# Optimization experiments

Hardware: AMD Instinct MI355X
Metric: run time of the kernel (lower is better)

The kernel has to match this reference:

```python
import jax, jax.numpy as jnp
import numpy as np

B, L, F, DM, H, DFF, NL, PRED = 8, 1000, 7, 512, 8, 2048, 4, 50
DK = DM // H           # head dim 64
P = DK // 4            # learned-mask proj dim 16
EPS = 1e-5
SCALE = 1.0 / float(np.sqrt(DK))


def _ln(x, g, b):
    m = jnp.mean(x, -1, keepdims=True)
    v = jnp.mean((x - m) ** 2, -1, keepdims=True)
    return (x - m) / jnp.sqrt(v + EPS) * g + b


def _make_pe():
    pos = np.arange(L, dtype=np.float32)[:, None]
    div = np.exp(np.arange(0, DM, 2, dtype=np.float32) * (-np.log(10000.0) / DM))
    pe = np.zeros((L, DM), dtype=np.float32)
    pe[:, 0::2] = np.sin(pos * div)
    pe[:, 1::2] = np.cos(pos * div)
    return jnp.asarray(pe)


def setup_inputs() -> dict:
    key = jax.random.key(0)
    ks = iter(jax.random.split(key, 40))
    def w(shape, s=0.02):
        return jax.random.normal(next(ks), shape, jnp.float32) * s
    return {
        "x": jax.random.normal(next(ks), (B, L, F), jnp.float32),
        "emb_w": w((F, DM)), "emb_b": jnp.zeros((DM,), jnp.float32),
        "pe": _make_pe(),
        "Wq": w((NL, DM, DM)), "bq": jnp.zeros((NL, DM), jnp.float32),
        "Wk": w((NL, DM, DM)), "bk": jnp.zeros((NL, DM), jnp.float32),
        "Wv": w((NL, DM, DM)), "bv": jnp.zeros((NL, DM), jnp.float32),
        "Wo": w((NL, DM, DM)), "bo": jnp.zeros((NL, DM), jnp.float32),
        "W1": w((NL, DM, DFF)), "b1": jnp.zeros((NL, DFF), jnp.float32),
        "W2": w((NL, DFF, DM)), "b2": jnp.zeros((NL, DM), jnp.float32),
        "g1": jnp.ones((NL, DM), jnp.float32), "be1": jnp.zeros((NL, DM), jnp.float32),
        "g2": jnp.ones((NL, DM), jnp.float32), "be2": jnp.zeros((NL, DM), jnp.float32),
        "lm_qw": w((DK, P)), "lm_qb": jnp.zeros((P,), jnp.float32),
        "lm_kw": w((DK, P)), "lm_kb": jnp.zeros((P,), jnp.float32),
        "gn": jnp.ones((DM,), jnp.float32), "bn": jnp.zeros((DM,), jnp.float32),
        "fc_w": w((DM, PRED)), "fc_b": jnp.zeros((PRED,), jnp.float32),
    }


def reference(x, emb_w, emb_b, pe, Wq, bq, Wk, bk, Wv, bv, Wo, bo,
              W1, b1, W2, b2, g1, be1, g2, be2,
              lm_qw, lm_qb, lm_kw, lm_kb, gn, bn, fc_w, fc_b):
    # eval mode: dropout = identity
    h = x @ emb_w + emb_b + pe[None]                 # [B,L,DM]
    for i in range(NL):
        q = (h @ Wq[i] + bq[i]).reshape(B, L, H, DK)
        k = (h @ Wk[i] + bk[i]).reshape(B, L, H, DK)
        v = (h @ Wv[i] + bv[i]).reshape(B, L, H, DK)
        scores = jnp.einsum('blhd,bshd->bhls', q, k) * SCALE
        # shared LearnedMask: per-head Q/K projection to P dims, tanh bias
        qp = q @ lm_qw + lm_qb                       # [B,L,H,P]
        kp = k @ lm_kw + lm_kb                       # [B,S,H,P]
        scores = scores + jnp.tanh(jnp.einsum('blhp,bshp->bhls', qp, kp))
        attn = jax.nn.softmax(scores, axis=-1)       # mask_flag=False: no mask
        ctx = jnp.einsum('bhls,bshd->blhd', attn, v).reshape(B, L, DM)
        h = _ln(h + ctx @ Wo[i] + bo[i], g1[i], be1[i])
        y = jax.nn.relu(h @ W1[i] + b1[i]) @ W2[i] + b2[i]
        h2 = _ln(h + y, g2[i], be2[i])
        h = _ln(h2 + y, g2[i], be2[i])               # module applies norm2 twice
    h = _ln(h, gn, bn)                               # Encoder final norm
    return h[:, -1, :] @ fc_w + fc_b                 # [B, PRED]
```

## Files before the change

### kernel.cpp

```cpp
#include <hip/hip_runtime.h>
#include <math.h>

#define B_    8
#define L_    1000
#define F_    7
#define DM_   512
#define H_    8
#define DFF_  2048
#define NL_   4
#define PRED_ 50
#define DK_   64
#define P_    16
#define EPS_  1e-5f
#define QKVS  1792

#define L2E_   1.4426950408889634f
#define C_QS   0.18033688011112042f
#define BS_QP  2.8853900817779268f
#define SHFT_  24.0f

typedef unsigned short u16;
typedef __bf16 bf16x8 __attribute__((ext_vector_type(8)));
typedef float  f32x4  __attribute__((ext_vector_type(4)));

__device__ inline float wave_reduce_sum(float x) {
#pragma unroll
  for (int off = 32; off >= 1; off >>= 1) x += __shfl_xor(x, off, 64);
  return x;
}
__device__ inline u16 f2bf(float f) {
  unsigned int u = __float_as_uint(f);
  unsigned int r = u + 0x7FFFu + ((u >> 16) & 1u);
  return (u16)(r >> 16);
}
__device__ inline unsigned int pack2(float a, float b) {
  return (unsigned int)f2bf(a) | ((unsigned int)f2bf(b) << 16);
}
__device__ inline float bf2f(u16 u) { return __uint_as_float(((unsigned int)u) << 16); }
__device__ inline float fexp2(float x) { return __builtin_amdgcn_exp2f(x); }
__device__ inline float frcp(float x) { return __builtin_amdgcn_rcpf(x); }

union bfrag { bf16x8 b; uint4 q; u16 u[8]; };

__device__ inline void gload16(const u16* g, u16* l) {
  __builtin_amdgcn_global_load_lds(
      (const __attribute__((address_space(1))) void*)g,
      (__attribute__((address_space(3))) void*)l, 16, 0, 0);
}

__global__ __launch_bounds__(256)
void transpose_w(const float* __restrict__ in, u16* __restrict__ out,
                 int K, int N, size_t in_lstride, size_t out_lstride,
                 int row_off, int out_ld) {
  __shared__ float tile[32][33];
  int z = blockIdx.z;
  int kk0 = blockIdx.y * 32, nn0 = blockIdx.x * 32;
  int tx = threadIdx.x & 31, ty = threadIdx.x >> 5;
  const float* ip = in + z * in_lstride;
  u16* op = out + z * out_lstride;
#pragma unroll
  for (int i = 0; i < 4; i++)
    tile[ty + i * 8][tx] = ip[(size_t)(kk0 + ty + i * 8) * N + nn0 + tx];
  __syncthreads();
#pragma unroll
  for (int i = 0; i < 4; i++)
    op[(size_t)(row_off + nn0 + ty + i * 8) * out_ld + kk0 + tx] = f2bf(tile[tx][ty + i * 8]);
}

__global__ __launch_bounds__(256)
void wfuse_kernel(const float* __restrict__ Wq, const float* __restrict__ Wk,
                  const float* __restrict__ lmqw, const float* __restrict__ lmkw,
                  u16* __restrict__ Wt) {
  int hh = blockIdx.x, side = blockIdx.y, layer = blockIdx.z;
  const float* W = (side ? Wk : Wq) + (size_t)layer * 512 * 512;
  const float* lw = side ? lmkw : lmqw;
  float scale = side ? 1.0f : BS_QP;
  __shared__ float lws[64][17];
  int t = threadIdx.x;
  for (int i = t; i < 1024; i += 256) lws[i >> 4][i & 15] = lw[i];
  __syncthreads();
  int p = t & 15, kk = t >> 4;
  u16* orow = Wt + (size_t)layer * QKVS * 512 + (size_t)(1536 + side * 128 + hh * 16 + p) * 512;
  for (int kb = 0; kb < 32; kb++) {
    int k = kb * 16 + kk;
    const float* wr = W + (size_t)k * 512 + hh * 64;
    float acc = 0.f;
#pragma unroll
    for (int d = 0; d < 64; d++) acc = fmaf(wr[d], lws[d][p], acc);
    orow[k] = f2bf(acc * scale);
  }
}

__global__ __launch_bounds__(256)
void concat_bias(const float* __restrict__ bq, const float* __restrict__ bk,
                 const float* __restrict__ bv,
                 const float* __restrict__ lmqw, const float* __restrict__ lmqb,
                 const float* __restrict__ lmkw, const float* __restrict__ lmkb,
                 float* __restrict__ bqkv) {
  int i = blockIdx.x * 256 + threadIdx.x;
  int l = i / QKVS, j = i % QKVS;
  float v;
  if (j < 512) v = bq[l * 512 + j];
  else if (j < 1024) v = bk[l * 512 + j - 512];
  else if (j < 1536) v = bv[l * 512 + j - 1024];
  else if (j < 1664) {
    int hh = (j - 1536) >> 4, p = (j - 1536) & 15;
    float acc = lmqb[p];
#pragma unroll
    for (int d = 0; d < 64; d++) acc = fmaf(bq[l * 512 + hh * 64 + d], lmqw[d * 16 + p], acc);
    v = acc * BS_QP;
  } else {
    int hh = (j - 1664) >> 4, p = (j - 1664) & 15;
    float acc = lmkb[p];
#pragma unroll
    for (int d = 0; d < 64; d++) acc = fmaf(bk[l * 512 + hh * 64 + d], lmkw[d * 16 + p], acc);
    v = acc;
  }
  bqkv[i] = v;
}

__global__ __launch_bounds__(512)
void embed_kernel(const float* __restrict__ x, const float* __restrict__ emb_w,
                  const float* __restrict__ emb_b, const float* __restrict__ pe,
                  u16* __restrict__ h16) {
  int bl = blockIdx.x;
  int l = bl % L_;
  int d = threadIdx.x;
  const float* xr = x + (size_t)bl * F_;
  float acc = emb_b[d] + pe[(size_t)l * DM_ + d];
#pragma unroll
  for (int f = 0; f < F_; f++) acc = fmaf(xr[f], emb_w[f * DM_ + d], acc);
  h16[(size_t)bl * DM_ + d] = f2bf(acc);
}

template<int BN>
__global__ __launch_bounds__(256)
void gemm16(const u16* __restrict__ A, const u16* __restrict__ Bt,
            const float* __restrict__ bias, const u16* __restrict__ resid,
            u16* __restrict__ C16, u16* __restrict__ vtg,
            int M, int K, int N, int relu, int nscale, float sval) {
  constexpr int NTW = BN / 32;
  constexpr int BG  = BN / 32;
  __shared__ u16 As[128 * 64];
  __shared__ u16 Bs[BN * 64];
  int t = threadIdx.x;
  int w = t >> 6, lane = t & 63;
  int wr = w >> 1, wc = w & 1;
  int mloc = lane & 15, quad = lane >> 4;
  int m0 = blockIdx.y * 128, n0 = blockIdx.x * BN;

  const u16* agp[4]; u16* alds[4];
#pragma unroll
  for (int j = 0; j < 4; j++) {
    int r = w * 32 + j * 8 + (lane >> 3);
    int gm = m0 + r; if (gm > M - 1) gm = M - 1;
    int ch = (lane & 7) ^ (r & 7);
    agp[j] = A + (size_t)gm * K + ch * 8;
    alds[j] = As + (w * 32 + j * 8) * 64;
  }
  const u16* bgp[BG]; u16* blds[BG];
#pragma unroll
  for (int j = 0; j < BG; j++) {
    int r = w * (8 * BG) + j * 8 + (lane >> 3);
    int ch = (lane & 7) ^ (r & 7);
    bgp[j] = Bt + (size_t)(n0 + r) * K + ch * 8;
    blds[j] = Bs + (w * (8 * BG) + j * 8) * 64;
  }
  const u16* apt[2][4];
#pragma unroll
  for (int mi = 0; mi < 4; mi++) {
    int tr = wr * 64 + mi * 16 + mloc;
    apt[0][mi] = As + tr * 64 + ((quad ^ (tr & 7)) * 8);
    apt[1][mi] = As + tr * 64 + (((4 + quad) ^ (tr & 7)) * 8);
  }
  const u16* bpt[2][NTW];
#pragma unroll
  for (int nt = 0; nt < NTW; nt++) {
    int tr = wc * (BN / 2) + nt * 16 + mloc;
    bpt[0][nt] = Bs + tr * 64 + ((quad ^ (tr & 7)) * 8);
    bpt[1][nt] = Bs + tr * 64 + (((4 + quad) ^ (tr & 7)) * 8);
  }

  f32x4 acc[4][NTW];
#pragma unroll
  for (int mi = 0; mi < 4; mi++)
#pragma unroll
    for (int nt = 0; nt < NTW; nt++) acc[mi][nt] = (f32x4){0.f, 0.f, 0.f, 0.f};

  for (int k0 = 0; k0 < K; k0 += 64) {
    __syncthreads();
#pragma unroll
    for (int j = 0; j < 4; j++) gload16(agp[j] + k0, alds[j]);
#pragma unroll
    for (int j = 0; j < BG; j++) gload16(bgp[j] + k0, blds[j]);
    __syncthreads();
#pragma unroll
    for (int kc = 0; kc < 2; kc++) {
      bf16x8 af[4], bv[NTW];
#pragma unroll
      for (int mi = 0; mi < 4; mi++) af[mi] = *(const bf16x8*)apt[kc][mi];
#pragma unroll
      for (int nt = 0; nt < NTW; nt++) bv[nt] = *(const bf16x8*)bpt[kc][nt];
#pragma unroll
      for (int mi = 0; mi < 4; mi++)
#pragma unroll
        for (int nt = 0; nt < NTW; nt++)
          acc[mi][nt] = __builtin_amdgcn_mfma_f32_16x16x32_bf16(af[mi], bv[nt], acc[mi][nt], 0, 0, 0);
    }
  }

#pragma unroll
  for (int mi = 0; mi < 4; mi++) {
    int m_r0 = m0 + wr * 64 + mi * 16 + quad * 4;
#pragma unroll
    for (int nt = 0; nt < NTW; nt++) {
      int nbase = n0 + wc * (BN / 2) + nt * 16;
      int n = nbase + mloc;
      if (vtg && nbase >= 1024 && nbase < 1536) {
        if (m_r0 < M) {
          int bb = (m_r0 * 67109) >> 26;
          int ll = m_r0 - bb * 1000;
          int hh2 = (n - 1024) >> 6, dk = n & 63;
          float bn_ = bias[n];
          union { uint2 d; u16 s[4]; } pk;
#pragma unroll
          for (int r = 0; r < 4; r++) pk.s[r] = f2bf(acc[mi][nt][r] + bn_);
          u16* dst = vtg + ((size_t)(bb * 8 + hh2) * 64 + dk) * 1024 + ll;
          *(uint2*)dst = pk.d;
        }
      } else {
        float bn_ = bias[n];
#pragma unroll
        for (int r = 0; r < 4; r++) {
          int m = m_r0 + r;
          if (m >= M) continue;
          size_t crow = (size_t)m * N;
          float vsum = acc[mi][nt][r] + bn_;
          if (resid) vsum += bf2f(resid[crow + n]);
          if (n < nscale) vsum *= sval;
          if (relu) vsum = fmaxf(vsum, 0.f);
          C16[crow + n] = f2bf(vsum);
        }
      }
    }
  }
}

#define KT   64
__global__ __launch_bounds__(256)
void attn_mfma_kernel(const u16* __restrict__ qkv, const u16* __restrict__ vtg,
                      u16* __restrict__ ctx) {
  __shared__ u16 Ks[2 * KT * 64];
  __shared__ u16 Vt[2 * 64 * KT];
  __shared__ u16 Kp[2 * KT * 16];

  int Lid = blockIdx.x;
  int qt = Lid >> 6;
  int bh = ((Lid & 7) << 3) | ((Lid >> 3) & 7);
  int b = bh >> 3, hh = bh & 7;
  int l0 = qt * 64;
  int t = threadIdx.x;
  int wv = t >> 6, lane = t & 63;
  int m = lane & 15, quad = lane >> 4;

  int lq = l0 + wv * 16 + m; if (lq > L_ - 1) lq = L_ - 1;
  const u16* qrow = qkv + (size_t)(b * L_ + lq) * QKVS + hh * DK_;
  bf16x8 qa0 = *(const bf16x8*)(qrow + quad * 8);
  bf16x8 qa1 = *(const bf16x8*)(qrow + 32 + quad * 8);
  bfrag qpa;
  if (quad < 2) {
    qpa.q = *(const uint4*)(qkv + (size_t)(b * L_ + lq) * QKVS + 1536 + hh * P_ + quad * 8);
  } else {
    qpa.q = make_uint4(0u, 0u, 0u, 0u);
  }

  const u16* ks_g = qkv + ((size_t)b * L_ + (t >> 3)) * QKVS + 512 + hh * DK_
                    + ((t & 7) ^ ((t >> 3) & 7)) * 8;
  u16* ks_l = Ks + wv * 512;
  const u16* vt_g = vtg + ((size_t)bh * DK_ + (t >> 3)) * 1024
                    + ((t & 7) ^ ((t >> 3) & 7)) * 8;
  u16* vt_l = Vt + wv * 512;
  const u16* kp_g = qkv + ((size_t)b * L_ + (t >> 1)) * QKVS + 1664 + hh * P_
                    + (t & 1) * 8;
  u16* kp_l = Kp + wv * 512;

  f32x4 O[4];
#pragma unroll
  for (int nt = 0; nt < 4; nt++) O[nt] = (f32x4){0.f, 0.f, 0.f, 0.f};
  float lsum = 0.f;
  const f32x4 zz = (f32x4){0.f, 0.f, 0.f, 0.f};

#pragma unroll
  for (int j = 0; j < 2; j++) {
    gload16(ks_g + (size_t)(j * 32) * QKVS, ks_l + j * 2048);
    gload16(vt_g + (size_t)j * 32 * 1024, vt_l + j * 2048);
  }
  if (wv < 2) gload16(kp_g, kp_l);
  __syncthreads();

  for (int tt = 0; tt < 16; ++tt) {
    const int s0 = tt * KT;
    const int c = tt & 1;
    if (tt < 15) {
      const int sn = s0 + KT, nb = c ^ 1;
#pragma unroll
      for (int j = 0; j < 2; j++) {
        gload16(ks_g + ((size_t)sn + j * 32) * QKVS, ks_l + nb * 4096 + j * 2048);
        gload16(vt_g + sn + (size_t)j * 32 * 1024, vt_l + nb * 4096 + j * 2048);
      }
      if (wv < 2) gload16(kp_g + (size_t)sn * QKVS, kp_l + nb * 1024);
    }

    const u16* Kc = Ks + c * 4096;
    const u16* Vc = Vt + c * 4096;
    const u16* Pc = Kp + c * 1024;

    unsigned pklo[4], pkhi[4];
#pragma unroll
    for (int nt = 0; nt < 4; nt++) {
      const u16* kb = Kc + (nt * 16 + m) * 64;
      int x0 = (quad ^ (m & 7)) * 8;
      int x1 = ((4 + quad) ^ (m & 7)) * 8;
      bf16x8 kf0 = *(const bf16x8*)(kb + x0);
      bf16x8 kf1 = *(const bf16x8*)(kb + x1);
      bf16x8 kpf = *(const bf16x8*)(Pc + (nt * 16 + m) * 16 + (quad & 1) * 8);
      __builtin_amdgcn_s_setprio(1);
      f32x4 sacc = __builtin_amdgcn_mfma_f32_16x16x32_bf16(kf0, qa0, zz, 0, 0, 0);
      sacc = __builtin_amdgcn_mfma_f32_16x16x32_bf16(kf1, qa1, sacc, 0, 0, 0);
      f32x4 macc = __builtin_amdgcn_mfma_f32_16x16x32_bf16(kpf, qpa.b, zz, 0, 0, 0);
      __builtin_amdgcn_s_setprio(0);
      int keyb = s0 + nt * 16 + quad * 4;
      float pv[4];
#pragma unroll
      for (int r = 0; r < 4; r++) {
        float e = fexp2(macc[r]);
        float d = frcp(e + 1.f);
        float th = fmaf(d, -2.f * L2E_, L2E_);
        float s = sacc[r] + th;
        if (keyb + r >= L_) s = -3e38f;
        float p = fexp2(s - SHFT_);
        pv[r] = p;
        lsum += p;
      }
      pklo[nt] = pack2(pv[0], pv[1]);
      pkhi[nt] = pack2(pv[2], pv[3]);
    }

#pragma unroll
    for (int ks = 0; ks < 2; ks++) {
      int sl = m + ((quad & 1) << 5);
      unsigned e0a = (unsigned)__shfl((int)pklo[2 * ks],     sl, 64);
      unsigned e0b = (unsigned)__shfl((int)pklo[2 * ks + 1], sl, 64);
      unsigned e1a = (unsigned)__shfl((int)pkhi[2 * ks],     sl, 64);
      unsigned e1b = (unsigned)__shfl((int)pkhi[2 * ks + 1], sl, 64);
      unsigned o0a = (unsigned)__shfl((int)pklo[2 * ks],     sl + 16, 64);
      unsigned o0b = (unsigned)__shfl((int)pklo[2 * ks + 1], sl + 16, 64);
      unsigned o1a = (unsigned)__shfl((int)pkhi[2 * ks],     sl + 16, 64);
      unsigned o1b = (unsigned)__shfl((int)pkhi[2 * ks + 1], sl + 16, 64);
      bool hi = quad >= 2;
      bfrag af;
      af.q.x = hi ? e0b : e0a;
      af.q.y = hi ? e1b : e1a;
      af.q.z = hi ? o0b : o0a;
      af.q.w = hi ? o1b : o1a;
      __builtin_amdgcn_s_setprio(1);
#pragma unroll
      for (int ntd = 0; ntd < 4; ntd++) {
        const u16* vb = Vc + (ntd * 16 + m) * KT + (((ks * 4 + quad) ^ (m & 7)) * 8);
        O[ntd] = __builtin_amdgcn_mfma_f32_16x16x32_bf16(af.b, *(const bf16x8*)vb, O[ntd], 0, 0, 0);
      }
      __builtin_amdgcn_s_setprio(0);
    }
    if (tt < 15) __syncthreads();
  }

  lsum += __shfl_xor(lsum, 16, 64);
  lsum += __shfl_xor(lsum, 32, 64);
#pragma unroll
  for (int r = 0; r < 4; r++) {
    int l = l0 + wv * 16 + quad * 4 + r;
    if (l >= L_) continue;
    float inv = frcp(__shfl(lsum, quad * 4 + r, 64));
    u16* crow = ctx + ((size_t)(b * L_ + l)) * DM_ + hh * DK_;
#pragma unroll
    for (int nt = 0; nt < 4; nt++) crow[nt * 16 + m] = f2bf(O[nt][r] * inv);
  }
}

__global__ __launch_bounds__(256)
void ln_kernel(const u16* __restrict__ a, const float* __restrict__ g,
               const float* __restrict__ be, u16* __restrict__ o) {
  int row = blockIdx.x;
  int t = threadIdx.x;
  size_t base = (size_t)row * DM_;
  unsigned int av = *(const unsigned int*)(a + base + 2 * t);
  float x0 = bf2f((u16)av), x1 = bf2f((u16)(av >> 16));
  float s = wave_reduce_sum(x0 + x1);
  float ss = wave_reduce_sum(x0 * x0 + x1 * x1);
  __shared__ float sh_s[4], sh_ss[4];
  int wv = t >> 6, lane = t & 63;
  if (lane == 0) { sh_s[wv] = s; sh_ss[wv] = ss; }
  __syncthreads();
  float S = sh_s[0] + sh_s[1] + sh_s[2] + sh_s[3];
  float SS = sh_ss[0] + sh_ss[1] + sh_ss[2] + sh_ss[3];
  float mean = S * (1.0f / DM_);
  float var = SS * (1.0f / DM_) - mean * mean;
  float rstd = rsqrtf(var + EPS_);
  float r0 = (x0 - mean) * rstd * g[2 * t] + be[2 * t];
  float r1 = (x1 - mean) * rstd * g[2 * t + 1] + be[2 * t + 1];
  *(unsigned int*)(o + base + 2 * t) = pack2(r0, r1);
}

__global__ __launch_bounds__(256)
void ln2x_kernel(const u16* __restrict__ hin, const u16* __restrict__ y,
                 const float* __restrict__ g, const float* __restrict__ be,
                 u16* __restrict__ o16) {
  int row = blockIdx.x;
  int t = threadIdx.x;
  size_t base = (size_t)row * DM_;
  unsigned int hv = *(const unsigned int*)(hin + base + 2 * t);
  unsigned int yv = *(const unsigned int*)(y + base + 2 * t);
  float y0 = bf2f((u16)yv), y1 = bf2f((u16)(yv >> 16));
  float x0 = bf2f((u16)hv) + y0, x1 = bf2f((u16)(hv >> 16)) + y1;
  __shared__ float sh_s[4], sh_ss[4];
  int wv = t >> 6, lane = t & 63;
  float g0 = g[2 * t], g1v = g[2 * t + 1], b0 = be[2 * t], b1v = be[2 * t + 1];

  float s = wave_reduce_sum(x0 + x1);
  float ss = wave_reduce_sum(x0 * x0 + x1 * x1);
  if (lane == 0) { sh_s[wv] = s; sh_ss[wv] = ss; }
  __syncthreads();
  float S = sh_s[0] + sh_s[1] + sh_s[2] + sh_s[3];
  float SS = sh_ss[0] + sh_ss[1] + sh_ss[2] + sh_ss[3];
  float mean = S * (1.0f / DM_);
  float var = SS * (1.0f / DM_) - mean * mean;
  float rstd = rsqrtf(var + EPS_);
  float h20 = (x0 - mean) * rstd * g0 + b0 + y0;
  float h21 = (x1 - mean) * rstd * g1v + b1v + y1;
  __syncthreads();

  s = wave_reduce_sum(h20 + h21);
  ss = wave_reduce_sum(h20 * h20 + h21 * h21);
  if (lane == 0) { sh_s[wv] = s; sh_ss[wv] = ss; }
  __syncthreads();
  S = sh_s[0] + sh_s[1] + sh_s[2] + sh_s[3];
  SS = sh_ss[0] + sh_ss[1] + sh_ss[2] + sh_ss[3];
  mean = S * (1.0f / DM_);
  var = SS * (1.0f / DM_) - mean * mean;
  rstd = rsqrtf(var + EPS_);
  float r0 = (h20 - mean) * rstd * g0 + b0;
  float r1 = (h21 - mean) * rstd * g1v + b1v;
  *(unsigned int*)(o16 + base + 2 * t) = pack2(r0, r1);
}

__global__ __launch_bounds__(512)
void final_kernel(const u16* __restrict__ h, const float* __restrict__ gn,
                  const float* __restrict__ bn, const float* __restrict__ fcw,
                  const float* __restrict__ fcb, float* __restrict__ out) {
  int b = blockIdx.x;
  int t = threadIdx.x;
  size_t base = ((size_t)b * L_ + (L_ - 1)) * DM_;
  float x = bf2f(h[base + t]);
  float s = wave_reduce_sum(x);
  float ss = wave_reduce_sum(x * x);
  __shared__ float sh_s[8], sh_ss[8];
  int wv = t >> 6, lane = t & 63;
  if (lane == 0) { sh_s[wv] = s; sh_ss[wv] = ss; }
  __syncthreads();
  float S = 0.f, SS = 0.f;
#pragma unroll
  for (int i = 0; i < 8; i++) { S += sh_s[i]; SS += sh_ss[i]; }
  float mean = S * (1.0f / DM_);
  float var = SS * (1.0f / DM_) - mean * mean;
  float rstd = rsqrtf(var + EPS_);
  __shared__ float hn[DM_];
  hn[t] = (x - mean) * rstd * gn[t] + bn[t];
  __syncthreads();
  if (t < PRED_) {
    float acc = fcb[t];
#pragma unroll 8
    for (int d = 0; d < DM_; d++) acc = fmaf(hn[d], fcw[d * PRED_ + t], acc);
    out[b * PRED_ + t] = acc;
  }
}

extern "C" void kernel_launch(void* const* d_in, const int* in_sizes, int n_in,
                              void* d_out, int out_size, void* d_ws, size_t ws_size,
                              hipStream_t stream) {
  const float* x     = (const float*)d_in[0];
  const float* emb_w = (const float*)d_in[1];
  const float* emb_b = (const float*)d_in[2];
  const float* pe    = (const float*)d_in[3];
  const float* Wq = (const float*)d_in[4];  const float* bq = (const float*)d_in[5];
  const float* Wk = (const float*)d_in[6];  const float* bk = (const float*)d_in[7];
  const float* Wv = (const float*)d_in[8];  const float* bv = (const float*)d_in[9];
  const float* Wo = (const float*)d_in[10]; const float* bo = (const float*)d_in[11];
  const float* W1 = (const float*)d_in[12]; const float* b1 = (const float*)d_in[13];
  const float* W2 = (const float*)d_in[14]; const float* b2 = (const float*)d_in[15];
  const float* g1 = (const float*)d_in[16]; const float* be1 = (const float*)d_in[17];
  const float* g2 = (const float*)d_in[18]; const float* be2 = (const float*)d_in[19];
  const float* lm_qw = (const float*)d_in[20]; const float* lm_qb = (const float*)d_in[21];
  const float* lm_kw = (const float*)d_in[22]; const float* lm_kb = (const float*)d_in[23];
  const float* gn = (const float*)d_in[24]; const float* bn = (const float*)d_in[25];
  const float* fc_w = (const float*)d_in[26]; const float* fc_b = (const float*)d_in[27];
  float* out = (float*)d_out;

  const size_t ROWS = (size_t)B_ * L_;
  u16* qkv16 = (u16*)d_ws;
  u16* ctx16 = qkv16 + ROWS * QKVS;
  u16* ffn1  = qkv16;
  u16* h16   = ctx16 + ROWS * DM_;
  u16* t16   = h16 + ROWS * DM_;
  u16* vtg   = t16 + ROWS * DM_;
  u16* Wqkv_t = vtg + (size_t)64 * 64 * 1024;
  u16* Wo_t   = Wqkv_t + (size_t)NL_ * QKVS * DM_;
  u16* W1_t   = Wo_t + (size_t)NL_ * DM_ * DM_;
  u16* W2_t   = W1_t + (size_t)NL_ * DFF_ * DM_;
  float* bqkv = (float*)(W2_t + (size_t)NL_ * DM_ * DFF_);

  transpose_w<<<dim3(16, 16, NL_), 256, 0, stream>>>(Wq, Wqkv_t, DM_, DM_, (size_t)DM_ * DM_, (size_t)QKVS * DM_, 0, DM_);
  transpose_w<<<dim3(16, 16, NL_), 256, 0, stream>>>(Wk, Wqkv_t, DM_, DM_, (size_t)DM_ * DM_, (size_t)QKVS * DM_, 512, DM_);
  transpose_w<<<dim3(16, 16, NL_), 256, 0, stream>>>(Wv, Wqkv_t, DM_, DM_, (size_t)DM_ * DM_, (size_t)QKVS * DM_, 1024, DM_);
  transpose_w<<<dim3(16, 16, NL_), 256, 0, stream>>>(Wo, Wo_t, DM_, DM_, (size_t)DM_ * DM_, (size_t)DM_ * DM_, 0, DM_);
  transpose_w<<<dim3(64, 16, NL_), 256, 0, stream>>>(W1, W1_t, DM_, DFF_, (size_t)DM_ * DFF_, (size_t)DFF_ * DM_, 0, DM_);
  transpose_w<<<dim3(16, 64, NL_), 256, 0, stream>>>(W2, W2_t, DFF_, DM_, (size_t)DFF_ * DM_, (size_t)DM_ * DFF_, 0, DFF_);
  wfuse_kernel<<<dim3(H_, 2, NL_), 256, 0, stream>>>(Wq, Wk, lm_qw, lm_kw, Wqkv_t);
  concat_bias<<<NL_ * QKVS / 256, 256, 0, stream>>>(bq, bk, bv, lm_qw, lm_qb, lm_kw, lm_kb, bqkv);

  embed_kernel<<<dim3((unsigned)ROWS), 512, 0, stream>>>(x, emb_w, emb_b, pe, h16);

  dim3 g_qkv(QKVS / 128, 63);
  dim3 g_ffn1(DFF_ / 128, 63);
  dim3 g_n512(DM_ / 64, 63);
  dim3 g_attn(1024);

  for (int i = 0; i < NL_; i++) {
    gemm16<128><<<g_qkv, 256, 0, stream>>>(h16, Wqkv_t + (size_t)i * QKVS * DM_,
        bqkv + i * QKVS, nullptr, qkv16, vtg, 8000, DM_, QKVS, 0, 512, C_QS);

    attn_mfma_kernel<<<g_attn, 256, 0, stream>>>(qkv16, vtg, ctx16);

    gemm16<64><<<g_n512, 256, 0, stream>>>(ctx16, Wo_t + (size_t)i * DM_ * DM_,
        bo + i * DM_, h16, t16, nullptr, 8000, DM_, DM_, 0, 0, 1.0f);
    ln_kernel<<<dim3((unsigned)ROWS), 256, 0, stream>>>(t16, g1 + i * DM_, be1 + i * DM_, h16);

    gemm16<128><<<g_ffn1, 256, 0, stream>>>(h16, W1_t + (size_t)i * DFF_ * DM_,
        b1 + i * DFF_, nullptr, ffn1, nullptr, 8000, DM_, DFF_, 1, 0, 1.0f);
    gemm16<64><<<g_n512, 256, 0, stream>>>(ffn1, W2_t + (size_t)i * DM_ * DFF_,
        b2 + i * DM_, nullptr, t16, nullptr, 8000, DFF_, DM_, 0, 0, 1.0f);

    ln2x_kernel<<<dim3((unsigned)ROWS), 256, 0, stream>>>(h16, t16, g2 + i * DM_, be2 + i * DM_, h16);
  }

  final_kernel<<<B_, 512, 0, stream>>>(h16, gn, bn, fc_w, fc_b, out);
}
```

Before: 1.131 ms.

## Double-buffer GEMM LDS tiles with K-step 32 to overlap loads and MFMA

The bf16 GEMM kernel now uses two LDS buffers, each holding a K=32 slice with two rows packed per 64-element LDS row under an XOR swizzle. The next slice is prefetched while MFMAs run on the current one, and there is one barrier per step instead of two. This aims to hide global-to-LDS load latency behind compute. In exchange there are twice as many loop iterations with smaller per-iteration work. Correctness of the single barrier depends on gload16 being synchronous register-staged loads or on ordering of the async LDS writes.

After: 1.157 ms. 2.3% more time.

```diff
diff --git a/kernel.cpp b/kernel.cpp
--- a/kernel.cpp
+++ b/kernel.cpp
@@ -140,45 +140,48 @@
             u16* __restrict__ C16, u16* __restrict__ vtg,
             int M, int K, int N, int relu, int nscale, float sval) {
   constexpr int NTW = BN / 32;
-  constexpr int BG  = BN / 32;
-  __shared__ u16 As[128 * 64];
-  __shared__ u16 Bs[BN * 64];
+  constexpr int AG  = 2;
+  constexpr int BG  = BN / 64;
+  constexpr int ASZ = 64 * 64;
+  constexpr int BSZ = (BN / 2) * 64;
+  __shared__ u16 As[2 * ASZ];
+  __shared__ u16 Bs[2 * BSZ];
   int t = threadIdx.x;
   int w = t >> 6, lane = t & 63;
   int wr = w >> 1, wc = w & 1;
   int mloc = lane & 15, quad = lane >> 4;
   int m0 = blockIdx.y * 128, n0 = blockIdx.x * BN;
 
-  const u16* agp[4]; u16* alds[4];
-#pragma unroll
-  for (int j = 0; j < 4; j++) {
-    int r = w * 32 + j * 8 + (lane >> 3);
-    int gm = m0 + r; if (gm > M - 1) gm = M - 1;
-    int ch = (lane & 7) ^ (r & 7);
-    agp[j] = A + (size_t)gm * K + ch * 8;
-    alds[j] = As + (w * 32 + j * 8) * 64;
+  const u16* agp[AG]; u16* alds[AG];
+#pragma unroll
+  for (int j = 0; j < AG; j++) {
+    int R = w * 16 + j * 8 + (lane >> 3);
+    int c = (lane & 7) ^ (R & 7);
+    int gm = m0 + 2 * R + (c >> 2); if (gm > M - 1) gm = M - 1;
+    agp[j] = A + (size_t)gm * K + (c & 3) * 8;
+    alds[j] = As + (w * 16 + j * 8) * 64;
   }
   const u16* bgp[BG]; u16* blds[BG];
 #pragma unroll
   for (int j = 0; j < BG; j++) {
-    int r = w * (8 * BG) + j * 8 + (lane >> 3);
-    int ch = (lane & 7) ^ (r & 7);
-    bgp[j] = Bt + (size_t)(n0 + r) * K + ch * 8;
+    int R = w * (8 * BG) + j * 8 + (lane >> 3);
+    int c = (lane & 7) ^ (R & 7);
+    bgp[j] = Bt + (size_t)(n0 + 2 * R + (c >> 2)) * K + (c & 3) * 8;
     blds[j] = Bs + (w * (8 * BG) + j * 8) * 64;
   }
-  const u16* apt[2][4];
+  const u16* apt[4];
 #pragma unroll
   for (int mi = 0; mi < 4; mi++) {
     int tr = wr * 64 + mi * 16 + mloc;
-    apt[0][mi] = As + tr * 64 + ((quad ^ (tr & 7)) * 8);
-    apt[1][mi] = As + tr * 64 + (((4 + quad) ^ (tr & 7)) * 8);
-  }
-  const u16* bpt[2][NTW];
+    int R = tr >> 1, c = (tr & 1) * 4 + quad;
+    apt[mi] = As + R * 64 + ((c ^ (R & 7)) * 8);
+  }
+  const u16* bpt[NTW];
 #pragma unroll
   for (int nt = 0; nt < NTW; nt++) {
     int tr = wc * (BN / 2) + nt * 16 + mloc;
-    bpt[0][nt] = Bs + tr * 64 + ((quad ^ (tr & 7)) * 8);
-    bpt[1][nt] = Bs + tr * 64 + (((4 + quad) ^ (tr & 7)) * 8);
+    int R = tr >> 1, c = (tr & 1) * 4 + quad;
+    bpt[nt] = Bs + R * 64 + ((c ^ (R & 7)) * 8);
   }
 
   f32x4 acc[4][NTW];
@@ -187,26 +190,36 @@
 #pragma unroll
     for (int nt = 0; nt < NTW; nt++) acc[mi][nt] = (f32x4){0.f, 0.f, 0.f, 0.f};
 
-  for (int k0 = 0; k0 < K; k0 += 64) {
-    __syncthreads();
-#pragma unroll
-    for (int j = 0; j < 4; j++) gload16(agp[j] + k0, alds[j]);
-#pragma unroll
-    for (int j = 0; j < BG; j++) gload16(bgp[j] + k0, blds[j]);
-    __syncthreads();
-#pragma unroll
-    for (int kc = 0; kc < 2; kc++) {
-      bf16x8 af[4], bv[NTW];
-#pragma unroll
-      for (int mi = 0; mi < 4; mi++) af[mi] = *(const bf16x8*)apt[kc][mi];
-#pragma unroll
-      for (int nt = 0; nt < NTW; nt++) bv[nt] = *(const bf16x8*)bpt[kc][nt];
-#pragma unroll
-      for (int mi = 0; mi < 4; mi++)
-#pragma unroll
-        for (int nt = 0; nt < NTW; nt++)
-          acc[mi][nt] = __builtin_amdgcn_mfma_f32_16x16x32_bf16(af[mi], bv[nt], acc[mi][nt], 0, 0, 0);
+#pragma unroll
+  for (int j = 0; j < AG; j++) gload16(agp[j], alds[j]);
+#pragma unroll
+  for (int j = 0; j < BG; j++) gload16(bgp[j], blds[j]);
+  __syncthreads();
+
+  const int nk = K >> 5;
+  int cur = 0;
+  for (int tt = 0; tt < nk; ++tt) {
+    if (tt + 1 < nk) {
+      const int nxt = cur ^ 1;
+      const int koff = (tt + 1) * 32;
+#pragma unroll
+      for (int j = 0; j < AG; j++) gload16(agp[j] + koff, alds[j] + nxt * ASZ);
+#pragma unroll
+      for (int j = 0; j < BG; j++) gload16(bgp[j] + koff, blds[j] + nxt * BSZ);
     }
+    const int ao = cur * ASZ, bo = cur * BSZ;
+    bf16x8 af[4], bv[NTW];
+#pragma unroll
+    for (int mi = 0; mi < 4; mi++) af[mi] = *(const bf16x8*)(apt[mi] + ao);
+#pragma unroll
+    for (int nt = 0; nt < NTW; nt++) bv[nt] = *(const bf16x8*)(bpt[nt] + bo);
+#pragma unroll
+    for (int mi = 0; mi < 4; mi++)
+#pragma unroll
+      for (int nt = 0; nt < NTW; nt++)
+        acc[mi][nt] = __builtin_amdgcn_mfma_f32_16x16x32_bf16(af[mi], bv[nt], acc[mi][nt], 0, 0, 0);
+    if (tt + 1 < nk) __syncthreads();
+    cur ^= 1;
   }
 
 #pragma unroll
```
